# Performance work log

Hardware: AMD Instinct MI355X
Metric: run time of the kernel (lower is better)

The kernel has to match this reference:

```python
import jax, jax.numpy as jnp
import numpy as np

DIM = 1024
NUM_HEADS = 16
HEAD_DIM = DIM // NUM_HEADS  # 64; only used for the softmax scale


def setup_inputs() -> dict:
    key = jax.random.key(0)
    ks = jax.random.split(key, 9)
    s = 1.0 / np.sqrt(DIM)
    return {
        "x": jax.random.normal(ks[0], (2, 4096, DIM), dtype=jnp.float32),
        "Wq": jax.random.normal(ks[1], (DIM, DIM), dtype=jnp.float32) * s,
        "bq": jnp.zeros((DIM,), dtype=jnp.float32),
        "Wk": jax.random.normal(ks[2], (DIM, DIM), dtype=jnp.float32) * s,
        "bk": jnp.zeros((DIM,), dtype=jnp.float32),
        "Wv": jax.random.normal(ks[3], (DIM, DIM), dtype=jnp.float32) * s,
        "bv": jnp.zeros((DIM,), dtype=jnp.float32),
        "Wo": jax.random.normal(ks[4], (DIM, DIM), dtype=jnp.float32) * s,
        "bo": jnp.zeros((DIM,), dtype=jnp.float32),
    }


def reference(x, Wq, bq, Wk, bk, Wv, bv, Wo, bo):
    # Projections (nn.Linear equivalents)
    q = jnp.einsum("bsd,df->bsf", x, Wq) + bq
    k = jnp.einsum("bsd,df->bsf", x, Wk) + bk
    v = jnp.einsum("bsd,df->bsf", x, Wv) + bv
    # Full-dim attention (no head split); scale uses head_dim per original code.
    scale = 1.0 / np.sqrt(HEAD_DIM)
    scores = jnp.einsum("bqd,bkd->bqk", q, k) * scale  # [B, S, S]
    attn = jax.nn.softmax(scores, axis=-1)
    out = jnp.einsum("bqk,bkd->bqd", attn, v)
    return jnp.einsum("bsd,df->bsf", out, Wo) + bo
```

## Files before the change

### kernel.cpp

```cpp
#include <hip/hip_runtime.h>

typedef unsigned short u16;
using bf16x8  = __attribute__((ext_vector_type(8))) __bf16;
using floatx4 = __attribute__((ext_vector_type(4))) float;

__device__ __forceinline__ u16 f2bf(float f) {
  unsigned int u = __builtin_bit_cast(unsigned int, f);
  u += 0x7fffu + ((u >> 16) & 1u);
  return (u16)(u >> 16);
}
__device__ __forceinline__ float bf2f(u16 h) {
  unsigned int u = ((unsigned int)h) << 16;
  return __builtin_bit_cast(float, u);
}

#define AS1(p) ((const __attribute__((address_space(1))) void*)(p))
#define AS3(p) ((__attribute__((address_space(3))) void*)(p))

#define GEMM_PROLOGUE_AT(bmv, bnv)                                           \
  __shared__ u16 As[128 * 32];                                               \
  __shared__ u16 Bs[128 * 32];                                               \
  const int tid  = threadIdx.x;                                              \
  const int wave = tid >> 6, lane = tid & 63;                                \
  const int wm = (wave >> 1) * 64, wn = (wave & 1) * 64;                     \
  const long bm = (bmv), bn = (bnv);                                         \
  floatx4 acc[4][4] = {};                                                    \
  const int srow = lane >> 2;                                                \
  const int scol = (lane & 3) * 8;                                           \
  const int c0 = wave * 2, c1 = c0 + 1;                                      \
  const int fr = lane & 15;                                                  \
  const int kq = (lane >> 4) * 8;                                            \
  const int oc = (lane >> 4) * 4;

#define GEMM_PROLOGUE() GEMM_PROLOGUE_AT((long)blockIdx.y * 128, (long)blockIdx.x * 128)

#define GEMM_STAGE(Ab, Bb, K, k0)                                            \
    __syncthreads();                                                         \
    __builtin_amdgcn_global_load_lds(AS1(Ab + (long)(c0*16 + srow)*K + k0 + scol), AS3(As + c0*512), 16, 0, 0); \
    __builtin_amdgcn_global_load_lds(AS1(Ab + (long)(c1*16 + srow)*K + k0 + scol), AS3(As + c1*512), 16, 0, 0); \
    __builtin_amdgcn_global_load_lds(AS1(Bb + (long)(c0*16 + srow)*K + k0 + scol), AS3(Bs + c0*512), 16, 0, 0); \
    __builtin_amdgcn_global_load_lds(AS1(Bb + (long)(c1*16 + srow)*K + k0 + scol), AS3(Bs + c1*512), 16, 0, 0); \
    __syncthreads();                                                         \
    bf16x8 af[4], bfv[4];                                                    \
    _Pragma("unroll")                                                        \
    for (int mi = 0; mi < 4; ++mi)                                           \
      af[mi] = *(const bf16x8*)(As + (wm + mi*16 + fr)*32 + kq);             \
    _Pragma("unroll")                                                        \
    for (int ni = 0; ni < 4; ++ni)                                           \
      bfv[ni] = *(const bf16x8*)(Bs + (wn + ni*16 + fr)*32 + kq);

#define GEMM_KSTEP(Ab, Bb, K, k0)                                            \
  {                                                                          \
    GEMM_STAGE(Ab, Bb, K, k0)                                                \
    _Pragma("unroll")                                                        \
    for (int mi = 0; mi < 4; ++mi)                                           \
      _Pragma("unroll")                                                      \
      for (int ni = 0; ni < 4; ++ni)                                         \
        acc[mi][ni] = __builtin_amdgcn_mfma_f32_16x16x32_bf16(af[mi], bfv[ni], acc[mi][ni], 0, 0, 0); \
  }

#define GEMM_KSTEP_SWAP(Ab, Bb, K, k0)                                       \
  {                                                                          \
    GEMM_STAGE(Ab, Bb, K, k0)                                                \
    _Pragma("unroll")                                                        \
    for (int mi = 0; mi < 4; ++mi)                                           \
      _Pragma("unroll")                                                      \
      for (int ni = 0; ni < 4; ++ni)                                         \
        acc[mi][ni] = __builtin_amdgcn_mfma_f32_16x16x32_bf16(bfv[ni], af[mi], acc[mi][ni], 0, 0, 0); \
  }

__global__ __launch_bounds__(256) void gemm_bt(
    const u16* __restrict__ A, const u16* __restrict__ Bt,
    float* __restrict__ Cout, const float* __restrict__ bias, int N, int K)
{
  GEMM_PROLOGUE();
  const u16* Ab = A + bm * K;
  const u16* Bb = Bt + bn * K;
  for (int k0 = 0; k0 < K; k0 += 32) GEMM_KSTEP_SWAP(Ab, Bb, K, k0);

#pragma unroll
  for (int mi = 0; mi < 4; ++mi) {
    long row = bm + wm + mi*16 + fr;
#pragma unroll
    for (int ni = 0; ni < 4; ++ni) {
      long colb = bn + wn + ni*16 + oc;
      float4 bv4 = *(const float4*)(bias + colb);
      float4 o;
      o.x = acc[mi][ni][0] + bv4.x;
      o.y = acc[mi][ni][1] + bv4.y;
      o.z = acc[mi][ni][2] + bv4.z;
      o.w = acc[mi][ni][3] + bv4.w;
      *(float4*)(Cout + row * N + colb) = o;
    }
  }
}

__global__ __launch_bounds__(256) void gemm_qk_exp(
    const u16* __restrict__ q, const u16* __restrict__ k,
    u16* __restrict__ probs, float* __restrict__ lpartT, float alpha)
{
  const int N = 4096, K = 1024;
  const int lin = blockIdx.x + (blockIdx.y << 5) + (blockIdx.z << 10);
  const int xcd = lin & 7, j = lin >> 3;
  const long b = xcd >> 2;
  const int band = (xcd & 3) * 8;
  const int t = j >> 6, w = j & 63;
  const int bx = t * 8 + (w & 7);
  const int by = band + (w >> 3);

  const u16* A  = q + b * 4096 * 1024;
  const u16* Bt = k + b * 4096 * 1024;
  u16* P = probs + b * 4096L * 4096;
  float* lp = lpartT + b * 4096 * 64;

  GEMM_PROLOGUE_AT((long)by * 128, (long)bx * 128);
  const u16* Ab = A + bm * K;
  const u16* Bb = Bt + bn * K;
  for (int k0 = 0; k0 < K; k0 += 32) GEMM_KSTEP_SWAP(Ab, Bb, K, k0);

  float rowsum[4] = {0.f, 0.f, 0.f, 0.f};
#pragma unroll
  for (int mi = 0; mi < 4; ++mi) {
    long row = bm + wm + mi*16 + fr;
#pragma unroll
    for (int ni = 0; ni < 4; ++ni) {
      long colb = bn + wn + ni*16 + oc;
      float e0 = __expf(acc[mi][ni][0] * alpha);
      float e1 = __expf(acc[mi][ni][1] * alpha);
      float e2 = __expf(acc[mi][ni][2] * alpha);
      float e3 = __expf(acc[mi][ni][3] * alpha);
      rowsum[mi] += (e0 + e1) + (e2 + e3);
      ushort4 o;
      o.x = f2bf(e0); o.y = f2bf(e1); o.z = f2bf(e2); o.w = f2bf(e3);
      *(ushort4*)(P + row * N + colb) = o;
    }
  }
  const long cg = bx * 2 + (wn >> 6);
#pragma unroll
  for (int mi = 0; mi < 4; ++mi) {
    float s = rowsum[mi];
    s += __shfl_xor(s, 16); s += __shfl_xor(s, 32);
    if (lane < 16)
      lp[(bm + wm + mi*16 + lane) * 64 + cg] = s;
  }
}

__global__ __launch_bounds__(256) void gemm_qkv(
    const u16* __restrict__ A, const u16* __restrict__ Bt,
    u16* __restrict__ qb, u16* __restrict__ kb, u16* __restrict__ vT,
    const float* __restrict__ bq, const float* __restrict__ bk,
    const float* __restrict__ bv)
{
  const int K = 1024;
  GEMM_PROLOGUE();
  const u16* Ab = A + bm * K;
  const u16* Bb = Bt + bn * K;

  if (bn < 2048) {
    for (int k0 = 0; k0 < K; k0 += 32) GEMM_KSTEP_SWAP(Ab, Bb, K, k0);
    u16* C = (bn < 1024) ? qb : kb;
    const float* bias = (bn < 1024) ? bq : bk;
#pragma unroll
    for (int mi = 0; mi < 4; ++mi) {
      long row = bm + wm + mi*16 + fr;
#pragma unroll
      for (int ni = 0; ni < 4; ++ni) {
        long colg = bn + wn + ni*16 + oc;
        long cc = colg & 1023;
        float4 bv4 = *(const float4*)(bias + cc);
        ushort4 o;
        o.x = f2bf(acc[mi][ni][0] + bv4.x);
        o.y = f2bf(acc[mi][ni][1] + bv4.y);
        o.z = f2bf(acc[mi][ni][2] + bv4.z);
        o.w = f2bf(acc[mi][ni][3] + bv4.w);
        *(ushort4*)(C + row * 1024 + cc) = o;
      }
    }
  } else {
    for (int k0 = 0; k0 < K; k0 += 32) GEMM_KSTEP(Ab, Bb, K, k0);
    const int orow = (lane >> 4) * 4;
    const int ocol = lane & 15;
#pragma unroll
    for (int ni = 0; ni < 4; ++ni) {
      long col = bn + wn + ni*16 + ocol;
      float bvv = bv[col - 2048];
#pragma unroll
      for (int mi = 0; mi < 4; ++mi) {
        long row = bm + wm + mi*16 + orow;
        long b_ = row >> 12, s = row & 4095, d = col - 2048;
        ushort4 o;
        o.x = f2bf(acc[mi][ni][0] + bvv);
        o.y = f2bf(acc[mi][ni][1] + bvv);
        o.z = f2bf(acc[mi][ni][2] + bvv);
        o.w = f2bf(acc[mi][ni][3] + bvv);
        *(ushort4*)(vT + b_ * (1024L * 4096) + d * 4096L + s) = o;
      }
    }
  }
}

__global__ __launch_bounds__(256) void gemm_pv_splitk(
    const u16* __restrict__ probs, const u16* __restrict__ vT,
    u16* __restrict__ pA, u16* __restrict__ pB)
{
  const int N = 1024, K = 4096, Ks = 1024;
  const int lin = blockIdx.x + (blockIdx.y << 3) + (blockIdx.z << 8);
  const int xcd = lin & 7, j = lin >> 3;
  const long b = xcd >> 2;
  const int sp = xcd & 3;
  const int bx = j & 7;
  const int by = j >> 3;

  const u16* A  = probs + b * 4096L * 4096;
  const u16* Bt = vT + b * 1024L * 4096;
  u16* part = (b ? pB : pA) + (long)sp * 4096 * 1024;

  GEMM_PROLOGUE_AT((long)by * 128, (long)bx * 128);
  const u16* Ab = A + bm * K;
  const u16* Bb = Bt + bn * K;
  const int kbeg = sp * Ks, kend = kbeg + Ks;
  for (int k0 = kbeg; k0 < kend; k0 += 32) GEMM_KSTEP_SWAP(Ab, Bb, K, k0);

#pragma unroll
  for (int mi = 0; mi < 4; ++mi) {
    long row = bm + wm + mi*16 + fr;
#pragma unroll
    for (int ni = 0; ni < 4; ++ni) {
      long colb = bn + wn + ni*16 + oc;
      ushort4 o;
      o.x = f2bf(acc[mi][ni][0]);
      o.y = f2bf(acc[mi][ni][1]);
      o.z = f2bf(acc[mi][ni][2]);
      o.w = f2bf(acc[mi][ni][3]);
      *(ushort4*)(part + row * N + colb) = o;
    }
  }
}

__global__ __launch_bounds__(256) void reduce4_div_row(
    const u16* __restrict__ pA, const u16* __restrict__ pB,
    const float* __restrict__ lpartT, u16* __restrict__ ob)
{
  const int row = blockIdx.x;
  const long b = blockIdx.y;
  const int tid = threadIdx.x;
  const u16* part = b ? pB : pA;
  const float* lp = lpartT + b * 4096 * 64;
  __shared__ float sl;
  if (tid < 64) {
    float s = lp[(long)row * 64 + tid];
#pragma unroll
    for (int off = 32; off; off >>= 1) s += __shfl_down(s, off);
    if (tid == 0) sl = s;
  }
  __syncthreads();
  const float inv = 1.0f / sl;
  const long base = (long)row * 1024 + tid * 4;
  float acc4[4] = {0.f, 0.f, 0.f, 0.f};
#pragma unroll
  for (int s = 0; s < 4; ++s) {
    ushort4 p = *(const ushort4*)(part + (long)s * 4096 * 1024 + base);
    acc4[0] += bf2f(p.x); acc4[1] += bf2f(p.y);
    acc4[2] += bf2f(p.z); acc4[3] += bf2f(p.w);
  }
  ushort4 o;
  o.x = f2bf(acc4[0] * inv);
  o.y = f2bf(acc4[1] * inv);
  o.z = f2bf(acc4[2] * inv);
  o.w = f2bf(acc4[3] * inv);
  *(ushort4*)(ob + b * 4096L * 1024 + base) = o;
}

__global__ __launch_bounds__(256) void prep(
    const float* __restrict__ x, u16* __restrict__ xb,
    const float* __restrict__ W0, const float* __restrict__ W1,
    const float* __restrict__ W2, const float* __restrict__ W3,
    u16* __restrict__ O0, u16* __restrict__ O1,
    u16* __restrict__ O2, u16* __restrict__ O3)
{
  __shared__ float tile[32][33];
  int blk = blockIdx.x;
  if (blk < 8192) {
    int i = blk * 256 + threadIdx.x;
    float4 f = ((const float4*)x)[i];
    ushort4 o;
    o.x = f2bf(f.x); o.y = f2bf(f.y); o.z = f2bf(f.z); o.w = f2bf(f.w);
    ((ushort4*)xb)[i] = o;
  } else {
    blk -= 8192;
    const int z = blk >> 10, t = blk & 1023;
    const float* in = (z == 0) ? W0 : (z == 1) ? W1 : (z == 2) ? W2 : W3;
    u16* outp = (z == 0) ? O0 : (z == 1) ? O1 : (z == 2) ? O2 : O3;
    const int bx = (t & 31) * 32, by = (t >> 5) * 32;
    const int tx = threadIdx.x & 31, ty = threadIdx.x >> 5;
    for (int i = ty; i < 32; i += 8)
      tile[i][tx] = in[(long)(by + i) * 1024 + bx + tx];
    __syncthreads();
    for (int i = ty; i < 32; i += 8)
      outp[(long)(bx + i) * 1024 + by + tx] = f2bf(tile[tx][i]);
  }
}

extern "C" void kernel_launch(void* const* d_in, const int* in_sizes, int n_in,
                              void* d_out, int out_size, void* d_ws, size_t ws_size,
                              hipStream_t stream) {
  const float* x  = (const float*)d_in[0];
  const float* Wq = (const float*)d_in[1];
  const float* bq = (const float*)d_in[2];
  const float* Wk = (const float*)d_in[3];
  const float* bk = (const float*)d_in[4];
  const float* Wv = (const float*)d_in[5];
  const float* bv = (const float*)d_in[6];
  const float* Wo = (const float*)d_in[7];
  const float* bo = (const float*)d_in[8];
  float* out = (float*)d_out;

  const int B = 2, S = 4096, D = 1024;
  const long MS = (long)B * S;
  const long MB = 1L << 20;

  char* w = (char*)d_ws;
  u16* qb  = (u16*)(w);
  u16* kb  = (u16*)(w + 16 * MB);
  u16* vT  = (u16*)(w + 32 * MB);
  u16* xb  = (u16*)(w + 48 * MB);
  u16* ob  = xb;
  u16* WqkvT = (u16*)(w + 64 * MB);
  u16* WoT = WqkvT + 3072L * 1024;
  u16* probs = (u16*)(w + 72 * MB);
  u16* partA = (u16*)(w);
  u16* partB = (u16*)(w + 136 * MB);
  float* lpartT = (float*)d_out;

  prep<<<dim3(8192 + 4096), 256, 0, stream>>>(
      x, xb, Wq, Wk, Wv, Wo,
      WqkvT, WqkvT + 1024L * 1024, WqkvT + 2048L * 1024, WoT);

  gemm_qkv<<<dim3(3 * D / 128, MS / 128), 256, 0, stream>>>(
      xb, WqkvT, qb, kb, vT, bq, bk, bv);

  const float scale = 0.125f;
  gemm_qk_exp<<<dim3(S / 128, S / 128, B), 256, 0, stream>>>(
      qb, kb, probs, lpartT, scale);
  gemm_pv_splitk<<<dim3(D / 128, S / 128, 8), 256, 0, stream>>>(
      probs, vT, partA, partB);
  reduce4_div_row<<<dim3(S, B), 256, 0, stream>>>(partA, partB, lpartT, ob);

  gemm_bt<<<dim3(D / 128, MS / 128), 256, 0, stream>>>(ob, WoT, out, bo, D, D);
}
```

Measured before the change: 409.2 us.

## Halve PV split-K slices, remap QKV blocks per XCD, use exp2 for softmax

The PV split-K drops from 4 slices to 2 per batch. Each block now covers 2048 of K, and the M rows are spread across XCD halves, so the reduce kernel only sums two partial buffers. The QKV GEMM grid is remapped so that each XCD handles a contiguous band of row tiles, which should improve L2 reuse of A. The exp in the QK kernel is replaced by hardware exp2 with a scale that folds in log2(e). The aim is less partial-buffer traffic and better cache locality, at the cost of fewer PV blocks and less parallelism there.

```diff
diff --git a/kernel.cpp b/kernel.cpp
--- a/kernel.cpp
+++ b/kernel.cpp
@@ -12,6 +12,13 @@
 __device__ __forceinline__ float bf2f(u16 h) {
   unsigned int u = ((unsigned int)h) << 16;
   return __builtin_bit_cast(float, u);
+}
+__device__ __forceinline__ float fast_exp2(float x) {
+#if __has_builtin(__builtin_amdgcn_exp2f)
+  return __builtin_amdgcn_exp2f(x);
+#else
+  return exp2f(x);
+#endif
 }
 
 #define AS1(p) ((const __attribute__((address_space(1))) void*)(p))
@@ -97,7 +104,7 @@
 
 __global__ __launch_bounds__(256) void gemm_qk_exp(
     const u16* __restrict__ q, const u16* __restrict__ k,
-    u16* __restrict__ probs, float* __restrict__ lpartT, float alpha)
+    u16* __restrict__ probs, float* __restrict__ lpartT, float alpha2)
 {
   const int N = 4096, K = 1024;
   const int lin = blockIdx.x + (blockIdx.y << 5) + (blockIdx.z << 10);
@@ -125,10 +132,10 @@
 #pragma unroll
     for (int ni = 0; ni < 4; ++ni) {
       long colb = bn + wn + ni*16 + oc;
-      float e0 = __expf(acc[mi][ni][0] * alpha);
-      float e1 = __expf(acc[mi][ni][1] * alpha);
-      float e2 = __expf(acc[mi][ni][2] * alpha);
-      float e3 = __expf(acc[mi][ni][3] * alpha);
+      float e0 = fast_exp2(acc[mi][ni][0] * alpha2);
+      float e1 = fast_exp2(acc[mi][ni][1] * alpha2);
+      float e2 = fast_exp2(acc[mi][ni][2] * alpha2);
+      float e3 = fast_exp2(acc[mi][ni][3] * alpha2);
       rowsum[mi] += (e0 + e1) + (e2 + e3);
       ushort4 o;
       o.x = f2bf(e0); o.y = f2bf(e1); o.z = f2bf(e2); o.w = f2bf(e3);
@@ -152,7 +159,12 @@
     const float* __restrict__ bv)
 {
   const int K = 1024;
-  GEMM_PROLOGUE();
+  const int lin = blockIdx.x + blockIdx.y * 24;
+  const int xcd = lin & 7, j = lin >> 3;
+  const int byl = j / 24, bx = j - byl * 24;
+  const int by = xcd * 8 + byl;
+
+  GEMM_PROLOGUE_AT((long)by * 128, (long)bx * 128);
   const u16* Ab = A + bm * K;
   const u16* Bb = Bt + bn * K;
 
@@ -203,13 +215,14 @@
     const u16* __restrict__ probs, const u16* __restrict__ vT,
     u16* __restrict__ pA, u16* __restrict__ pB)
 {
-  const int N = 1024, K = 4096, Ks = 1024;
+  const int N = 1024, K = 4096, Ks = 2048;
   const int lin = blockIdx.x + (blockIdx.y << 3) + (blockIdx.z << 8);
   const int xcd = lin & 7, j = lin >> 3;
-  const long b = xcd >> 2;
-  const int sp = xcd & 3;
+  const int slice = xcd >> 1, half = xcd & 1;
+  const long b = slice >> 1;
+  const int sp = slice & 1;
   const int bx = j & 7;
-  const int by = j >> 3;
+  const int by = (j >> 3) * 2 + half;
 
   const u16* A  = probs + b * 4096L * 4096;
   const u16* Bt = vT + b * 1024L * 4096;
@@ -237,7 +250,7 @@
   }
 }
 
-__global__ __launch_bounds__(256) void reduce4_div_row(
+__global__ __launch_bounds__(256) void reduce2_div_row(
     const u16* __restrict__ pA, const u16* __restrict__ pB,
     const float* __restrict__ lpartT, u16* __restrict__ ob)
 {
@@ -256,18 +269,13 @@
   __syncthreads();
   const float inv = 1.0f / sl;
   const long base = (long)row * 1024 + tid * 4;
-  float acc4[4] = {0.f, 0.f, 0.f, 0.f};
-#pragma unroll
-  for (int s = 0; s < 4; ++s) {
-    ushort4 p = *(const ushort4*)(part + (long)s * 4096 * 1024 + base);
-    acc4[0] += bf2f(p.x); acc4[1] += bf2f(p.y);
-    acc4[2] += bf2f(p.z); acc4[3] += bf2f(p.w);
-  }
+  ushort4 p0 = *(const ushort4*)(part + base);
+  ushort4 p1 = *(const ushort4*)(part + 4096L * 1024 + base);
   ushort4 o;
-  o.x = f2bf(acc4[0] * inv);
-  o.y = f2bf(acc4[1] * inv);
-  o.z = f2bf(acc4[2] * inv);
-  o.w = f2bf(acc4[3] * inv);
+  o.x = f2bf((bf2f(p0.x) + bf2f(p1.x)) * inv);
+  o.y = f2bf((bf2f(p0.y) + bf2f(p1.y)) * inv);
+  o.z = f2bf((bf2f(p0.z) + bf2f(p1.z)) * inv);
+  o.w = f2bf((bf2f(p0.w) + bf2f(p1.w)) * inv);
   *(ushort4*)(ob + b * 4096L * 1024 + base) = o;
 }
 
@@ -339,12 +347,12 @@
   gemm_qkv<<<dim3(3 * D / 128, MS / 128), 256, 0, stream>>>(
       xb, WqkvT, qb, kb, vT, bq, bk, bv);
 
-  const float scale = 0.125f;
+  const float scale2 = 0.125f * 1.44269504f;
   gemm_qk_exp<<<dim3(S / 128, S / 128, B), 256, 0, stream>>>(
-      qb, kb, probs, lpartT, scale);
-  gemm_pv_splitk<<<dim3(D / 128, S / 128, 8), 256, 0, stream>>>(
+      qb, kb, probs, lpartT, scale2);
+  gemm_pv_splitk<<<dim3(D / 128, S / 128, 4), 256, 0, stream>>>(
       probs, vT, partA, partB);
-  reduce4_div_row<<<dim3(S, B), 256, 0, stream>>>(partA, partB, lpartT, ob);
+  reduce2_div_row<<<dim3(S, B), 256, 0, stream>>>(partA, partB, lpartT, ob);
 
   gemm_bt<<<dim3(D / 128, MS / 128), 256, 0, stream>>>(ob, WoT, out, bo, D, D);
 }
```

After: 417.4 us. Within noise of the previous version (+2.0%).
